# Optimization experiments

Measured on AMD Instinct MI355X. Metric: run time of the kernel, lower is better.

## Reference

```python
import jax, jax.numpy as jnp
import numpy as np

D_MODEL = 1024
N_HEADS = 16
HEAD_DIM = D_MODEL // N_HEADS


def setup_inputs() -> dict:
    key = jax.random.key(0)
    ks = jax.random.split(key, 5)
    B, T = 4, 2048
    x = jax.random.normal(ks[0], (B, T, D_MODEL), dtype=jnp.float32)
    s_in = 1.0 / np.sqrt(D_MODEL)
    W_qkv = jax.random.normal(ks[1], (D_MODEL, 3 * D_MODEL), dtype=jnp.float32) * s_in
    b_qkv = jnp.zeros((3 * D_MODEL,), dtype=jnp.float32)
    W_proj = jax.random.normal(ks[2], (D_MODEL, D_MODEL), dtype=jnp.float32) * s_in
    b_proj = jnp.zeros((D_MODEL,), dtype=jnp.float32)
    return {"x": x, "W_qkv": W_qkv, "b_qkv": b_qkv, "W_proj": W_proj, "b_proj": b_proj}


def reference(x, W_qkv, b_qkv, W_proj, b_proj):
    B, T, C = x.shape
    qkv = x @ W_qkv + b_qkv                       # [B, T, 3C]
    q, k, v = jnp.split(qkv, 3, axis=-1)
    def heads(t):  # [B, T, C] -> [B, H, T, Dh]
        return t.reshape(B, T, N_HEADS, HEAD_DIM).transpose(0, 2, 1, 3)
    q, k, v = heads(q), heads(k), heads(v)
    scale = 1.0 / np.sqrt(HEAD_DIM)
    att = jnp.einsum('bhqd,bhkd->bhqk', q, k) * scale   # [B, H, T, T]
    causal = jnp.tril(jnp.ones((T, T), dtype=bool))
    att = jnp.where(causal, att, -jnp.inf)
    att = jax.nn.softmax(att, axis=-1)
    out = jnp.einsum('bhqk,bhkd->bhqd', att, v)          # [B, H, T, Dh]
    out = out.transpose(0, 2, 1, 3).reshape(B, T, C)
    return out @ W_proj + b_proj
```

## Files before the change

### kernel.cpp

```cpp
#include <hip/hip_runtime.h>
#include <hip/hip_bf16.h>

#define NH 16
#define HD 64
#define T_SEQ 2048
#define DM 1024

typedef __attribute__((ext_vector_type(8))) short short8;
typedef __attribute__((ext_vector_type(4))) short sh4;
typedef __attribute__((ext_vector_type(4))) float f32x4;
typedef __attribute__((ext_vector_type(16))) float f32x16;
typedef unsigned short ushort;

static __device__ __forceinline__ ushort f2bf(float f) {
    union { float f; unsigned int u; } c; c.f = f;
    unsigned int r = (c.u + 0x7fffu + ((c.u >> 16) & 1u)) >> 16;
    return (ushort)r;
}

static __device__ __forceinline__ void gload16(const ushort* g, ushort* l) {
    __builtin_amdgcn_global_load_lds(
        (const __attribute__((address_space(1))) void*)(const void*)g,
        (__attribute__((address_space(3))) void*)(void*)l, 16, 0, 0);
}

__global__ __launch_bounds__(256) void prep(const float* __restrict__ X,
                                            ushort* __restrict__ Xb,
                                            const float* __restrict__ W,
                                            ushort* __restrict__ Wt) {
    __shared__ float Ts[64][65];
    const int tid = threadIdx.x;
    if (blockIdx.x < 4096) {
        int i = blockIdx.x * 256 + tid;
        const float* s = X + (size_t)i * 8;
        float4 a = *(const float4*)(s);
        float4 b = *(const float4*)(s + 4);
        short8 o;
        o[0] = f2bf(a.x); o[1] = f2bf(a.y); o[2] = f2bf(a.z); o[3] = f2bf(a.w);
        o[4] = f2bf(b.x); o[5] = f2bf(b.y); o[6] = f2bf(b.z); o[7] = f2bf(b.w);
        *(short8*)(Xb + (size_t)i * 8) = o;
    } else {
        const int bid = blockIdx.x - 4096;
        const int N = 3 * DM;
        const int n0 = (bid % 48) * 64, k0 = (bid / 48) * 64;
        const int cg = tid & 15, r4 = tid >> 4;
        #pragma unroll
        for (int i = 0; i < 4; ++i) {
            int r = r4 + i * 16;
            float4 v = *(const float4*)(W + (size_t)(k0 + r) * N + n0 + cg * 4);
            Ts[r][cg * 4 + 0] = v.x; Ts[r][cg * 4 + 1] = v.y;
            Ts[r][cg * 4 + 2] = v.z; Ts[r][cg * 4 + 3] = v.w;
        }
        __syncthreads();
        #pragma unroll
        for (int i = 0; i < 4; ++i) {
            int r = r4 + i * 16;
            sh4 o;
            o[0] = (short)f2bf(Ts[cg * 4 + 0][r]);
            o[1] = (short)f2bf(Ts[cg * 4 + 1][r]);
            o[2] = (short)f2bf(Ts[cg * 4 + 2][r]);
            o[3] = (short)f2bf(Ts[cg * 4 + 3][r]);
            *(sh4*)(Wt + (size_t)(n0 + r) * DM + k0 + cg * 4) = o;
        }
    }
}

__global__ __launch_bounds__(256) void transpose_w(const float* __restrict__ W,
                                                   ushort* __restrict__ Wt, int N) {
    __shared__ float Ts[64][65];
    const int n0 = blockIdx.x * 64, k0 = blockIdx.y * 64;
    const int tid = threadIdx.x;
    const int cg = tid & 15, r4 = tid >> 4;
    #pragma unroll
    for (int i = 0; i < 4; ++i) {
        int r = r4 + i * 16;
        float4 v = *(const float4*)(W + (size_t)(k0 + r) * N + n0 + cg * 4);
        Ts[r][cg * 4 + 0] = v.x; Ts[r][cg * 4 + 1] = v.y;
        Ts[r][cg * 4 + 2] = v.z; Ts[r][cg * 4 + 3] = v.w;
    }
    __syncthreads();
    #pragma unroll
    for (int i = 0; i < 4; ++i) {
        int r = r4 + i * 16;
        sh4 o;
        o[0] = (short)f2bf(Ts[cg * 4 + 0][r]);
        o[1] = (short)f2bf(Ts[cg * 4 + 1][r]);
        o[2] = (short)f2bf(Ts[cg * 4 + 2][r]);
        o[3] = (short)f2bf(Ts[cg * 4 + 3][r]);
        *(sh4*)(Wt + (size_t)(n0 + r) * DM + k0 + cg * 4) = o;
    }
}

static __device__ __forceinline__ void gemm_core(
    const ushort* __restrict__ A, const ushort* __restrict__ Bt,
    ushort* __restrict__ smem, int m0, int n0, f32x4 acc[4][4])
{
    const int tid = threadIdx.x;
    const int wid = tid >> 6, lane = tid & 63;
    const int lr = lane & 15, g = lane >> 4;
    const int wm = wid >> 1, wn = wid & 1;
    const int lrow = lane >> 3, lslot = lane & 7;

    auto stage = [&](int b, int kt) {
        ushort* As = smem + b * 16384;
        ushort* Bs = As + 8192;
        #pragma unroll
        for (int i = 0; i < 4; ++i) {
            const int row = wid * 32 + i * 8 + lrow;
            const int gcol = (lslot ^ (row & 7)) * 8;
            const int ldsoff = (wid * 32 + i * 8) * 64;
            gload16(A  + (size_t)(m0 + row) * DM + kt * 64 + gcol, As + ldsoff);
            gload16(Bt + (size_t)(n0 + row) * DM + kt * 64 + gcol, Bs + ldsoff);
        }
    };

    stage(0, 0);
    #pragma unroll 1
    for (int kt = 0; kt < 16; ++kt) {
        const int cur = kt & 1;
        if (kt < 15) {
            stage(cur ^ 1, kt + 1);
            asm volatile("s_waitcnt vmcnt(8)" ::: "memory");
        } else {
            asm volatile("s_waitcnt vmcnt(0)" ::: "memory");
        }
        __builtin_amdgcn_s_barrier();
        __builtin_amdgcn_sched_barrier(0);
        const ushort* As = smem + cur * 16384;
        const ushort* Bs = As + 8192;
        #pragma unroll
        for (int ks = 0; ks < 2; ++ks) {
            short8 af[4], bfr[4];
            #pragma unroll
            for (int mi = 0; mi < 4; ++mi) {
                int row = wm * 64 + mi * 16 + lr;
                af[mi] = *(const short8*)(As + row * 64 + (((ks * 4 + g) ^ (row & 7)) * 8));
            }
            #pragma unroll
            for (int ni = 0; ni < 4; ++ni) {
                int row = wn * 64 + ni * 16 + lr;
                bfr[ni] = *(const short8*)(Bs + row * 64 + (((ks * 4 + g) ^ (row & 7)) * 8));
            }
            #pragma unroll
            for (int mi = 0; mi < 4; ++mi)
                #pragma unroll
                for (int ni = 0; ni < 4; ++ni)
                    acc[mi][ni] = __builtin_amdgcn_mfma_f32_16x16x32_bf16(af[mi], bfr[ni], acc[mi][ni], 0, 0, 0);
        }
        __builtin_amdgcn_sched_barrier(0);
        __builtin_amdgcn_s_barrier();
    }
}

__global__ __launch_bounds__(256) void qkv_mfma(
    const ushort* __restrict__ Xb, const ushort* __restrict__ Wqt,
    const float* __restrict__ bias,
    ushort* __restrict__ Qb, ushort* __restrict__ Kb, ushort* __restrict__ Vt)
{
    __shared__ __align__(16) ushort smem[32768];
    const int lin = blockIdx.x + 24 * blockIdx.y;
    const int swz = (lin & 7) * 192 + (lin >> 3);
    const int m0 = (swz / 24) * 128;
    const int n0 = (swz % 24) * 128;
    f32x4 acc[4][4] = {};
    gemm_core(Xb, Wqt, smem, m0, n0, acc);

    const int tid = threadIdx.x;
    const int wid = tid >> 6, lane = tid & 63;
    const int lr = lane & 15, g = lane >> 4;
    const int wm = wid >> 1, wn = wid & 1;
    const int which = n0 >> 10;
    const int bq = m0 >> 11;

    if (which < 2) {
        ushort* dst = which ? Kb : Qb;
        const float sc = which ? 1.0f : 0.125f * 1.44269504f;
        #pragma unroll
        for (int ni = 0; ni < 4; ++ni) {
            int nn = n0 + wn * 64 + ni * 16 + lr;
            const float bv = bias[nn];
            const int hh = (nn & 1023) >> 6, dd = nn & 63;
            const size_t hb = ((size_t)(bq * NH + hh)) * T_SEQ;
            #pragma unroll
            for (int mi = 0; mi < 4; ++mi)
                #pragma unroll
                for (int r = 0; r < 4; ++r) {
                    int t = (m0 + wm * 64 + mi * 16 + g * 4 + r) & 2047;
                    dst[(hb + t) * HD + dd] = f2bf((acc[mi][ni][r] + bv) * sc);
                }
        }
    } else {
        __syncthreads();
        ushort* Ct = smem;
        #pragma unroll
        for (int ni = 0; ni < 4; ++ni) {
            int lcol = wn * 64 + ni * 16 + lr;
            const float bv = bias[n0 + lcol];
            #pragma unroll
            for (int mi = 0; mi < 4; ++mi)
                #pragma unroll
                for (int r = 0; r < 4; ++r)
                    Ct[(wm * 64 + mi * 16 + g * 4 + r) * 128 + lcol] = f2bf(acc[mi][ni][r] + bv);
        }
        __syncthreads();
        const int dloc = tid >> 1, th = (tid & 1) * 64;
        const int nn = (n0 & 1023) + dloc;
        ushort* dst = Vt + ((size_t)(bq * 1024 + nn)) * T_SEQ + (m0 & 2047) + th;
        #pragma unroll
        for (int e8 = 0; e8 < 8; ++e8) {
            short8 v;
            #pragma unroll
            for (int u = 0; u < 8; ++u) v[u] = (short)Ct[(th + e8 * 8 + u) * 128 + dloc];
            *(short8*)(dst + e8 * 8) = v;
        }
    }
}

__global__ __launch_bounds__(256) void proj_mfma(
    const ushort* __restrict__ AO, const ushort* __restrict__ Wpt,
    const float* __restrict__ bias, float* __restrict__ Y)
{
    __shared__ __align__(16) ushort smem[32768];
    const int lin = blockIdx.x + 8 * blockIdx.y;
    const int swz = (lin & 7) * 64 + (lin >> 3);
    const int m0 = (swz >> 3) * 128;
    const int n0 = (swz & 7) * 128;
    f32x4 acc[4][4] = {};
    gemm_core(AO, Wpt, smem, m0, n0, acc);

    const int tid = threadIdx.x;
    const int wid = tid >> 6, lane = tid & 63;
    const int lr = lane & 15, g = lane >> 4;
    const int wm = wid >> 1, wn = wid & 1;
    #pragma unroll
    for (int ni = 0; ni < 4; ++ni) {
        int nn = n0 + wn * 64 + ni * 16 + lr;
        const float bv = bias[nn];
        #pragma unroll
        for (int mi = 0; mi < 4; ++mi)
            #pragma unroll
            for (int r = 0; r < 4; ++r) {
                int m = m0 + wm * 64 + mi * 16 + g * 4 + r;
                Y[(size_t)m * DM + nn] = acc[mi][ni][r] + bv;
            }
    }
}

__global__ __launch_bounds__(256) void attn_mfma(
    const ushort* __restrict__ Qb,
    const ushort* __restrict__ Kb,
    const ushort* __restrict__ Vt,
    ushort* __restrict__ AO)
{
    __shared__ __align__(16) ushort Ks[2][4096];
    __shared__ __align__(16) ushort Vs[2][4096];

    const int bh = blockIdx.x;
    const int j = 15 - blockIdx.y;
    const int tid = threadIdx.x;
    const int wid = tid >> 6;
    const int lane = tid & 63;
    const int ql = lane & 31;
    const int hi = lane >> 5;

    const ushort* Kg = Kb + (size_t)bh * T_SEQ * HD;
    const ushort* Vg = Vt + (size_t)bh * HD * T_SEQ;

    const int srow = tid >> 3;
    const int sco = (tid & 7) * 8;
    const int ssw = sco ^ ((srow & 7) << 3);
    const int sdst0 = srow * 64 + ssw;
    const int sdst1 = (srow + 32) * 64 + ssw;

    const int b = bh >> 4, h = bh & 15;
    ushort* AOg = AO + (size_t)b * T_SEQ * DM + h * HD;

    const int q0 = j * 128;
    const int qlo = q0 + wid * 32;
    const int ntiles = 2 * j + 2;

    short8 qb[4];
    {
        const ushort* Qg = Qb + ((size_t)bh * T_SEQ + qlo) * HD;
        #pragma unroll
        for (int ds = 0; ds < 4; ++ds)
            qb[ds] = *(const short8*)(Qg + (size_t)ql * HD + ds * 16 + hi * 8);
    }

    f32x16 po[2] = {};
    float lp = 0.f;

    short8 rk0, rk1, rv0, rv1;
    rk0 = *(const short8*)(Kg + (size_t)srow * HD + sco);
    rk1 = *(const short8*)(Kg + (size_t)(srow + 32) * HD + sco);
    rv0 = *(const short8*)(Vg + (size_t)srow * T_SEQ + sco);
    rv1 = *(const short8*)(Vg + (size_t)(srow + 32) * T_SEQ + sco);
    *(short8*)(&Ks[0][sdst0]) = rk0;  *(short8*)(&Ks[0][sdst1]) = rk1;
    *(short8*)(&Vs[0][sdst0]) = rv0;  *(short8*)(&Vs[0][sdst1]) = rv1;
    {
        const int nk0 = 64;
        rk0 = *(const short8*)(Kg + (size_t)(nk0 + srow) * HD + sco);
        rk1 = *(const short8*)(Kg + (size_t)(nk0 + srow + 32) * HD + sco);
        rv0 = *(const short8*)(Vg + (size_t)srow * T_SEQ + nk0 + sco);
        rv1 = *(const short8*)(Vg + (size_t)(srow + 32) * T_SEQ + nk0 + sco);
    }
    __syncthreads();

    for (int tt = 0; tt < ntiles; ++tt) {
        const int k0 = tt * 64;
        const int cur = tt & 1;
        if (tt + 1 < ntiles) {
            const int nxt = cur ^ 1;
            *(short8*)(&Ks[nxt][sdst0]) = rk0;  *(short8*)(&Ks[nxt][sdst1]) = rk1;
            *(short8*)(&Vs[nxt][sdst0]) = rv0;  *(short8*)(&Vs[nxt][sdst1]) = rv1;
            if (tt + 2 < ntiles) {
                const int nk0 = (tt + 2) * 64;
                rk0 = *(const short8*)(Kg + (size_t)(nk0 + srow) * HD + sco);
                rk1 = *(const short8*)(Kg + (size_t)(nk0 + srow + 32) * HD + sco);
                rv0 = *(const short8*)(Vg + (size_t)srow * T_SEQ + nk0 + sco);
                rv1 = *(const short8*)(Vg + (size_t)(srow + 32) * T_SEQ + nk0 + sco);
            }
        }

        if (k0 <= qlo + 31) {
            const ushort* ksb = Ks[cur];
            const ushort* vsb = Vs[cur];

            short8 vf[2][4];
            #pragma unroll
            for (int db = 0; db < 2; ++db)
                #pragma unroll
                for (int sl = 0; sl < 4; ++sl) {
                    int row = db * 32 + ql;
                    int slot = (sl * 2 + hi) ^ (row & 7);
                    vf[db][sl] = *(const short8*)(&vsb[row * 64 + slot * 8]);
                }

            f32x16 sp[2] = {};
            __builtin_amdgcn_s_setprio(1);
            #pragma unroll
            for (int kb = 0; kb < 2; ++kb) {
                #pragma unroll
                for (int ds = 0; ds < 4; ++ds) {
                    int row = kb * 32 + ql;
                    int slot = (ds * 2 + hi) ^ (row & 7);
                    short8 kf = *(const short8*)(&ksb[row * 64 + slot * 8]);
                    sp[kb] = __builtin_amdgcn_mfma_f32_32x32x16_bf16(kf, qb[ds], sp[kb], 0, 0, 0);
                }
            }
            __builtin_amdgcn_s_setprio(0);

            if (k0 + 63 > qlo) {
                #pragma unroll
                for (int kb = 0; kb < 2; ++kb) {
                    const int lim = qlo + ql - k0 - kb * 32 - 4 * hi;
                    #pragma unroll
                    for (int r = 0; r < 16; ++r) {
                        const int c = (r & 3) + 8 * (r >> 2);
                        sp[kb][r] = (c <= lim) ? sp[kb][r] : -INFINITY;
                    }
                }
            }

            float rs = 0.f;
            #pragma unroll
            for (int kb = 0; kb < 2; ++kb)
                #pragma unroll
                for (int r = 0; r < 16; ++r) {
                    float p;
                    asm("v_exp_f32 %0, %1" : "=v"(p) : "v"(sp[kb][r]));
                    sp[kb][r] = p;
                    rs += p;
                }
            lp += rs;

            #pragma unroll
            for (int kb = 0; kb < 2; ++kb) {
                #pragma unroll
                for (int ks16 = 0; ks16 < 2; ++ks16) {
                    unsigned int x0, x1, y0, y1;
                    const int rb0 = ks16 * 2, rb1 = ks16 * 2 + 1;
                    asm("v_cvt_pk_bf16_f32 %0, %1, %2" : "=v"(x0)
                        : "v"(sp[kb][4 * rb0 + 0]), "v"(sp[kb][4 * rb0 + 1]));
                    asm("v_cvt_pk_bf16_f32 %0, %1, %2" : "=v"(x1)
                        : "v"(sp[kb][4 * rb0 + 2]), "v"(sp[kb][4 * rb0 + 3]));
                    asm("v_cvt_pk_bf16_f32 %0, %1, %2" : "=v"(y0)
                        : "v"(sp[kb][4 * rb1 + 0]), "v"(sp[kb][4 * rb1 + 1]));
                    asm("v_cvt_pk_bf16_f32 %0, %1, %2" : "=v"(y1)
                        : "v"(sp[kb][4 * rb1 + 2]), "v"(sp[kb][4 * rb1 + 3]));
                    asm("v_permlane32_swap_b32 %0, %1" : "+v"(x0), "+v"(y0));
                    asm("v_permlane32_swap_b32 %0, %1" : "+v"(x1), "+v"(y1));
                    union { unsigned int w[4]; short8 s8; } pb;
                    pb.w[0] = x0; pb.w[1] = x1; pb.w[2] = y0; pb.w[3] = y1;
                    const int sl = kb * 2 + ks16;
                    __builtin_amdgcn_s_setprio(1);
                    po[0] = __builtin_amdgcn_mfma_f32_32x32x16_bf16(vf[0][sl], pb.s8, po[0], 0, 0, 0);
                    po[1] = __builtin_amdgcn_mfma_f32_32x32x16_bf16(vf[1][sl], pb.s8, po[1], 0, 0, 0);
                    __builtin_amdgcn_s_setprio(0);
                }
            }
        }
        __syncthreads();
    }

    lp += __shfl_xor(lp, 32);
    const float inv = 1.f / lp;
    const int q = qlo + ql;
    #pragma unroll
    for (int db = 0; db < 2; ++db) {
        #pragma unroll
        for (int rb = 0; rb < 4; ++rb) {
            unsigned int w0, w1;
            float f0 = po[db][4 * rb + 0] * inv, f1 = po[db][4 * rb + 1] * inv;
            float f2 = po[db][4 * rb + 2] * inv, f3 = po[db][4 * rb + 3] * inv;
            asm("v_cvt_pk_bf16_f32 %0, %1, %2" : "=v"(w0) : "v"(f0), "v"(f1));
            asm("v_cvt_pk_bf16_f32 %0, %1, %2" : "=v"(w1) : "v"(f2), "v"(f3));
            uint2 wv; wv.x = w0; wv.y = w1;
            *(uint2*)(AOg + (size_t)q * DM + db * 32 + 8 * rb + 4 * hi) = wv;
        }
    }
}

extern "C" void kernel_launch(void* const* d_in, const int* in_sizes, int n_in,
                              void* d_out, int out_size, void* d_ws, size_t ws_size,
                              hipStream_t stream) {
    const float* x      = (const float*)d_in[0];
    const float* W_qkv  = (const float*)d_in[1];
    const float* b_qkv  = (const float*)d_in[2];
    const float* W_proj = (const float*)d_in[3];
    const float* b_proj = (const float*)d_in[4];
    float* out = (float*)d_out;

    const size_t perbuf = (size_t)4 * NH * T_SEQ * HD;
    ushort* Qb  = (ushort*)d_ws;
    ushort* Kb  = Qb + perbuf;
    ushort* Vt  = Kb + perbuf;
    ushort* AO  = Vt + perbuf;
    ushort* Wqt = AO;
    ushort* Wpt = Qb;
    ushort* Xb  = (ushort*)d_out;

    hipLaunchKernelGGL(prep, dim3(4096 + 768), dim3(256), 0, stream, x, Xb, W_qkv, Wqt);
    hipLaunchKernelGGL(qkv_mfma, dim3(24, 64), dim3(256), 0, stream,
                       Xb, Wqt, b_qkv, Qb, Kb, Vt);
    hipLaunchKernelGGL(attn_mfma, dim3(64, 16), dim3(256), 0, stream,
                       Qb, Kb, Vt, AO);
    hipLaunchKernelGGL(transpose_w, dim3(16, 16), dim3(256), 0, stream, W_proj, Wpt, DM);
    hipLaunchKernelGGL(proj_mfma, dim3(8, 64), dim3(256), 0, stream,
                       AO, Wpt, b_proj, out);
}
```

Baseline: 155.0 us.

## Load K/V fragments directly from global into registers, dropping LDS staging

Removes the shared-memory double buffer and block-wide barriers from the attention kernel. Each wave now loads its own K and V MFMA fragments straight from global memory, with K prefetched one tile ahead in registers through ping-pong buffers. Each wave also computes its own tile count, so waves stop at their own causal limit instead of iterating with the block. This removes LDS traffic and synchronization, but the four waves now fetch the same K/V separately, which raises global/L2 traffic and register pressure.

```diff
diff --git a/kernel.cpp b/kernel.cpp
--- a/kernel.cpp
+++ b/kernel.cpp
@@ -252,9 +252,6 @@
     const ushort* __restrict__ Vt,
     ushort* __restrict__ AO)
 {
-    __shared__ __align__(16) ushort Ks[2][4096];
-    __shared__ __align__(16) ushort Vs[2][4096];
-
     const int bh = blockIdx.x;
     const int j = 15 - blockIdx.y;
     const int tid = threadIdx.x;
@@ -263,21 +260,15 @@
     const int ql = lane & 31;
     const int hi = lane >> 5;
 
-    const ushort* Kg = Kb + (size_t)bh * T_SEQ * HD;
-    const ushort* Vg = Vt + (size_t)bh * HD * T_SEQ;
-
-    const int srow = tid >> 3;
-    const int sco = (tid & 7) * 8;
-    const int ssw = sco ^ ((srow & 7) << 3);
-    const int sdst0 = srow * 64 + ssw;
-    const int sdst1 = (srow + 32) * 64 + ssw;
-
     const int b = bh >> 4, h = bh & 15;
     ushort* AOg = AO + (size_t)b * T_SEQ * DM + h * HD;
 
     const int q0 = j * 128;
     const int qlo = q0 + wid * 32;
-    const int ntiles = 2 * j + 2;
+    const int ntiles = (qlo >> 6) + 1;
+
+    const ushort* Kl = Kb + (size_t)bh * T_SEQ * HD + (size_t)ql * HD + hi * 8;
+    const ushort* Vl = Vt + (size_t)bh * HD * T_SEQ + (size_t)ql * T_SEQ + hi * 8;
 
     short8 qb[4];
     {
@@ -290,117 +281,92 @@
     f32x16 po[2] = {};
     float lp = 0.f;
 
-    short8 rk0, rk1, rv0, rv1;
-    rk0 = *(const short8*)(Kg + (size_t)srow * HD + sco);
-    rk1 = *(const short8*)(Kg + (size_t)(srow + 32) * HD + sco);
-    rv0 = *(const short8*)(Vg + (size_t)srow * T_SEQ + sco);
-    rv1 = *(const short8*)(Vg + (size_t)(srow + 32) * T_SEQ + sco);
-    *(short8*)(&Ks[0][sdst0]) = rk0;  *(short8*)(&Ks[0][sdst1]) = rk1;
-    *(short8*)(&Vs[0][sdst0]) = rv0;  *(short8*)(&Vs[0][sdst1]) = rv1;
-    {
-        const int nk0 = 64;
-        rk0 = *(const short8*)(Kg + (size_t)(nk0 + srow) * HD + sco);
-        rk1 = *(const short8*)(Kg + (size_t)(nk0 + srow + 32) * HD + sco);
-        rv0 = *(const short8*)(Vg + (size_t)srow * T_SEQ + nk0 + sco);
-        rv1 = *(const short8*)(Vg + (size_t)(srow + 32) * T_SEQ + nk0 + sco);
-    }
-    __syncthreads();
-
-    for (int tt = 0; tt < ntiles; ++tt) {
-        const int k0 = tt * 64;
-        const int cur = tt & 1;
-        if (tt + 1 < ntiles) {
-            const int nxt = cur ^ 1;
-            *(short8*)(&Ks[nxt][sdst0]) = rk0;  *(short8*)(&Ks[nxt][sdst1]) = rk1;
-            *(short8*)(&Vs[nxt][sdst0]) = rv0;  *(short8*)(&Vs[nxt][sdst1]) = rv1;
-            if (tt + 2 < ntiles) {
-                const int nk0 = (tt + 2) * 64;
-                rk0 = *(const short8*)(Kg + (size_t)(nk0 + srow) * HD + sco);
-                rk1 = *(const short8*)(Kg + (size_t)(nk0 + srow + 32) * HD + sco);
-                rv0 = *(const short8*)(Vg + (size_t)srow * T_SEQ + nk0 + sco);
-                rv1 = *(const short8*)(Vg + (size_t)(srow + 32) * T_SEQ + nk0 + sco);
-            }
-        }
-
-        if (k0 <= qlo + 31) {
-            const ushort* ksb = Ks[cur];
-            const ushort* vsb = Vs[cur];
-
-            short8 vf[2][4];
-            #pragma unroll
-            for (int db = 0; db < 2; ++db)
-                #pragma unroll
-                for (int sl = 0; sl < 4; ++sl) {
-                    int row = db * 32 + ql;
-                    int slot = (sl * 2 + hi) ^ (row & 7);
-                    vf[db][sl] = *(const short8*)(&vsb[row * 64 + slot * 8]);
-                }
-
-            f32x16 sp[2] = {};
-            __builtin_amdgcn_s_setprio(1);
+    auto loadK = [&](short8 (&kf)[2][4], int t) {
+        const int k0 = t * 64;
+        #pragma unroll
+        for (int kb = 0; kb < 2; ++kb)
+            #pragma unroll
+            for (int ds = 0; ds < 4; ++ds)
+                kf[kb][ds] = *(const short8*)(Kl + (size_t)(k0 + kb * 32) * HD + ds * 16);
+    };
+
+    auto body = [&](int t, short8 (&kcur)[2][4], short8 (&knxt)[2][4]) {
+        const int k0 = t * 64;
+        if (t + 1 < ntiles) loadK(knxt, t + 1);
+        short8 vf[2][4];
+        #pragma unroll
+        for (int db = 0; db < 2; ++db)
+            #pragma unroll
+            for (int sl = 0; sl < 4; ++sl)
+                vf[db][sl] = *(const short8*)(Vl + (size_t)(db * 32) * T_SEQ + k0 + sl * 16);
+
+        f32x16 sp[2] = {};
+        __builtin_amdgcn_s_setprio(1);
+        #pragma unroll
+        for (int kb = 0; kb < 2; ++kb)
+            #pragma unroll
+            for (int ds = 0; ds < 4; ++ds)
+                sp[kb] = __builtin_amdgcn_mfma_f32_32x32x16_bf16(kcur[kb][ds], qb[ds], sp[kb], 0, 0, 0);
+        __builtin_amdgcn_s_setprio(0);
+
+        if (k0 + 63 > qlo) {
             #pragma unroll
             for (int kb = 0; kb < 2; ++kb) {
-                #pragma unroll
-                for (int ds = 0; ds < 4; ++ds) {
-                    int row = kb * 32 + ql;
-                    int slot = (ds * 2 + hi) ^ (row & 7);
-                    short8 kf = *(const short8*)(&ksb[row * 64 + slot * 8]);
-                    sp[kb] = __builtin_amdgcn_mfma_f32_32x32x16_bf16(kf, qb[ds], sp[kb], 0, 0, 0);
-                }
-            }
-            __builtin_amdgcn_s_setprio(0);
-
-            if (k0 + 63 > qlo) {
-                #pragma unroll
-                for (int kb = 0; kb < 2; ++kb) {
-                    const int lim = qlo + ql - k0 - kb * 32 - 4 * hi;
-                    #pragma unroll
-                    for (int r = 0; r < 16; ++r) {
-                        const int c = (r & 3) + 8 * (r >> 2);
-                        sp[kb][r] = (c <= lim) ? sp[kb][r] : -INFINITY;
-                    }
-                }
-            }
-
-            float rs = 0.f;
-            #pragma unroll
-            for (int kb = 0; kb < 2; ++kb)
+                const int lim = qlo + ql - k0 - kb * 32 - 4 * hi;
                 #pragma unroll
                 for (int r = 0; r < 16; ++r) {
-                    float p;
-                    asm("v_exp_f32 %0, %1" : "=v"(p) : "v"(sp[kb][r]));
-                    sp[kb][r] = p;
-                    rs += p;
+                    const int c = (r & 3) + 8 * (r >> 2);
+                    sp[kb][r] = (c <= lim) ? sp[kb][r] : -INFINITY;
                 }
-            lp += rs;
-
-            #pragma unroll
-            for (int kb = 0; kb < 2; ++kb) {
-                #pragma unroll
-                for (int ks16 = 0; ks16 < 2; ++ks16) {
-                    unsigned int x0, x1, y0, y1;
-                    const int rb0 = ks16 * 2, rb1 = ks16 * 2 + 1;
-                    asm("v_cvt_pk_bf16_f32 %0, %1, %2" : "=v"(x0)
-                        : "v"(sp[kb][4 * rb0 + 0]), "v"(sp[kb][4 * rb0 + 1]));
-                    asm("v_cvt_pk_bf16_f32 %0, %1, %2" : "=v"(x1)
-                        : "v"(sp[kb][4 * rb0 + 2]), "v"(sp[kb][4 * rb0 + 3]));
-                    asm("v_cvt_pk_bf16_f32 %0, %1, %2" : "=v"(y0)
-                        : "v"(sp[kb][4 * rb1 + 0]), "v"(sp[kb][4 * rb1 + 1]));
-                    asm("v_cvt_pk_bf16_f32 %0, %1, %2" : "=v"(y1)
-                        : "v"(sp[kb][4 * rb1 + 2]), "v"(sp[kb][4 * rb1 + 3]));
-                    asm("v_permlane32_swap_b32 %0, %1" : "+v"(x0), "+v"(y0));
-                    asm("v_permlane32_swap_b32 %0, %1" : "+v"(x1), "+v"(y1));
-                    union { unsigned int w[4]; short8 s8; } pb;
-                    pb.w[0] = x0; pb.w[1] = x1; pb.w[2] = y0; pb.w[3] = y1;
-                    const int sl = kb * 2 + ks16;
-                    __builtin_amdgcn_s_setprio(1);
-                    po[0] = __builtin_amdgcn_mfma_f32_32x32x16_bf16(vf[0][sl], pb.s8, po[0], 0, 0, 0);
-                    po[1] = __builtin_amdgcn_mfma_f32_32x32x16_bf16(vf[1][sl], pb.s8, po[1], 0, 0, 0);
-                    __builtin_amdgcn_s_setprio(0);
-                }
-            }
-        }
-        __syncthreads();
+            }
+        }
+
+        float rs = 0.f;
+        #pragma unroll
+        for (int kb = 0; kb < 2; ++kb)
+            #pragma unroll
+            for (int r = 0; r < 16; ++r) {
+                float p;
+                asm("v_exp_f32 %0, %1" : "=v"(p) : "v"(sp[kb][r]));
+                sp[kb][r] = p;
+                rs += p;
+            }
+        lp += rs;
+
+        #pragma unroll
+        for (int kb = 0; kb < 2; ++kb) {
+            #pragma unroll
+            for (int ks16 = 0; ks16 < 2; ++ks16) {
+                unsigned int x0, x1, y0, y1;
+                const int rb0 = ks16 * 2, rb1 = ks16 * 2 + 1;
+                asm("v_cvt_pk_bf16_f32 %0, %1, %2" : "=v"(x0)
+                    : "v"(sp[kb][4 * rb0 + 0]), "v"(sp[kb][4 * rb0 + 1]));
+                asm("v_cvt_pk_bf16_f32 %0, %1, %2" : "=v"(x1)
+                    : "v"(sp[kb][4 * rb0 + 2]), "v"(sp[kb][4 * rb0 + 3]));
+                asm("v_cvt_pk_bf16_f32 %0, %1, %2" : "=v"(y0)
+                    : "v"(sp[kb][4 * rb1 + 0]), "v"(sp[kb][4 * rb1 + 1]));
+                asm("v_cvt_pk_bf16_f32 %0, %1, %2" : "=v"(y1)
+                    : "v"(sp[kb][4 * rb1 + 2]), "v"(sp[kb][4 * rb1 + 3]));
+                asm("v_permlane32_swap_b32 %0, %1" : "+v"(x0), "+v"(y0));
+                asm("v_permlane32_swap_b32 %0, %1" : "+v"(x1), "+v"(y1));
+                union { unsigned int w[4]; short8 s8; } pb;
+                pb.w[0] = x0; pb.w[1] = x1; pb.w[2] = y0; pb.w[3] = y1;
+                const int sl = kb * 2 + ks16;
+                __builtin_amdgcn_s_setprio(1);
+                po[0] = __builtin_amdgcn_mfma_f32_32x32x16_bf16(vf[0][sl], pb.s8, po[0], 0, 0, 0);
+                po[1] = __builtin_amdgcn_mfma_f32_32x32x16_bf16(vf[1][sl], pb.s8, po[1], 0, 0, 0);
+                __builtin_amdgcn_s_setprio(0);
+            }
+        }
+    };
+
+    short8 kA[2][4], kB[2][4];
+    loadK(kA, 0);
+    int tt = 0;
+    #pragma unroll 1
+    while (tt < ntiles) {
+        body(tt, kA, kB); ++tt;
+        if (tt < ntiles) { body(tt, kB, kA); ++tt; }
     }
 
     lp += __shfl_xor(lp, 32);
```

After: 221.7 us. 1.43x slower.
